# Kernel optimization log

Hardware: AMD Instinct MI355X
Metric: run time of the kernel (lower is better)

## Reference

```python
import jax, jax.numpy as jnp
import numpy as np

T = 200                      # TRAIN_ROIS_PER_IMAGE
RATIO = 0.33                 # ROI_POSITIVE_RATIO
P_MAX = int(T * RATIO)       # max positive ROIs (66)
MH, MW = 28, 28              # MASK_SHAPE
STD = jnp.array([0.1, 0.1, 0.2, 0.2], jnp.float32)  # BBOX_STD_DEV
EPS = 1e-6


def _iou(a, b):
    # a [N,4], b [G,4] -> [N,G] IoU (same math as overlaps_graph, without tiling)
    ay1, ax1, ay2, ax2 = a[:, 0:1], a[:, 1:2], a[:, 2:3], a[:, 3:4]
    by1, bx1, by2, bx2 = b[None, :, 0], b[None, :, 1], b[None, :, 2], b[None, :, 3]
    iy = jnp.maximum(jnp.minimum(ay2, by2) - jnp.maximum(ay1, by1), 0.0)
    ix = jnp.maximum(jnp.minimum(ax2, bx2) - jnp.maximum(ax1, bx1), 0.0)
    inter = iy * ix
    union = (ay2 - ay1) * (ax2 - ax1) + (by2 - by1) * (bx2 - bx1) - inter
    return inter / jnp.maximum(union, EPS)


def _box_refinement(box, gt):
    # standard Mask R-CNN box_refinement_graph
    h = jnp.maximum(box[:, 2] - box[:, 0], EPS)
    w = jnp.maximum(box[:, 3] - box[:, 1], EPS)
    cy = box[:, 0] + 0.5 * h
    cx = box[:, 1] + 0.5 * w
    gh = jnp.maximum(gt[:, 2] - gt[:, 0], EPS)
    gw = jnp.maximum(gt[:, 3] - gt[:, 1], EPS)
    gcy = gt[:, 0] + 0.5 * gh
    gcx = gt[:, 1] + 0.5 * gw
    return jnp.stack([(gcy - cy) / h, (gcx - cx) / w,
                      jnp.log(gh / h), jnp.log(gw / w)], axis=-1)


def _crop_and_resize(imgs, boxes):
    # imgs [T,H,W], boxes [T,4] normalized; TF crop_and_resize bilinear semantics,
    # extrapolation_value = 0 for samples outside [0, H-1] x [0, W-1].
    Tn, H, W = imgs.shape
    y1, x1, y2, x2 = boxes[:, 0], boxes[:, 1], boxes[:, 2], boxes[:, 3]
    iy = jnp.arange(MH, dtype=jnp.float32)
    ix = jnp.arange(MW, dtype=jnp.float32)
    ys = y1[:, None] * (H - 1) + iy[None, :] * ((y2 - y1) * (H - 1) / (MH - 1))[:, None]  # [T,MH]
    xs = x1[:, None] * (W - 1) + ix[None, :] * ((x2 - x1) * (W - 1) / (MW - 1))[:, None]  # [T,MW]
    y0 = jnp.floor(ys); x0 = jnp.floor(xs)
    wy = (ys - y0)[:, :, None]
    wx = (xs - x0)[:, None, :]
    y0i = jnp.clip(y0, 0, H - 1).astype(jnp.int32)
    y1i = jnp.clip(y0 + 1, 0, H - 1).astype(jnp.int32)
    x0i = jnp.clip(x0, 0, W - 1).astype(jnp.int32)
    x1i = jnp.clip(x0 + 1, 0, W - 1).astype(jnp.int32)
    t = jnp.arange(Tn)[:, None, None]
    v00 = imgs[t, y0i[:, :, None], x0i[:, None, :]]
    v01 = imgs[t, y0i[:, :, None], x1i[:, None, :]]
    v10 = imgs[t, y1i[:, :, None], x0i[:, None, :]]
    v11 = imgs[t, y1i[:, :, None], x1i[:, None, :]]
    val = (v00 * (1 - wx) + v01 * wx) * (1 - wy) + (v10 * (1 - wx) + v11 * wx) * wy
    ok = ((ys >= 0) & (ys <= H - 1))[:, :, None] & ((xs >= 0) & (xs <= W - 1))[:, None, :]
    return jnp.where(ok, val, 0.0)


def _targets_one(proposals, class_ids, boxes, masks):
    # proposals [N,4], class_ids [G] int, boxes [G,4], masks [H,W,G]
    N = proposals.shape[0]
    # zero-padding trim expressed as validity masks (jit-friendly fixed shapes)
    valid_prop = jnp.any(proposals != 0, axis=1)
    valid_gt = jnp.any(boxes != 0, axis=1)
    non_crowd = (class_ids > 0) & valid_gt
    crowd = (class_ids < 0) & valid_gt

    ov = _iou(proposals, boxes)                              # [N,G]
    ov_nc = jnp.where(non_crowd[None, :], ov, -1.0)          # mask crowd/padded gt
    roi_iou_max = ov_nc.max(axis=1)
    crowd_max = jnp.where(crowd[None, :], ov, 0.0).max(axis=1)

    pos_mask = valid_prop & (roi_iou_max >= 0.5)
    neg_mask = valid_prop & (roi_iou_max < 0.5) & (crowd_max < 0.001)

    # deterministic selection (original uses tf.random.shuffle): positives first-in-order
    pos_order = jnp.argsort(jnp.where(pos_mask, 0, 1))
    neg_order = jnp.argsort(jnp.where(neg_mask, 0, 1))
    pos_count = jnp.minimum(pos_mask.sum(), P_MAX)
    neg_needed = jnp.floor(pos_count.astype(jnp.float32) / RATIO).astype(jnp.int32) - pos_count
    neg_count = jnp.minimum(jnp.minimum(neg_needed, neg_mask.sum()), T - pos_count)

    slot = jnp.arange(T)
    is_pos = slot < pos_count
    is_neg = (slot >= pos_count) & (slot < pos_count + neg_count)
    src = jnp.where(is_pos,
                    pos_order[jnp.clip(slot, 0, N - 1)],
                    neg_order[jnp.clip(slot - pos_count, 0, N - 1)])
    rois = jnp.where((is_pos | is_neg)[:, None], proposals[src], 0.0)

    assign = jnp.argmax(ov_nc[src], axis=1)                  # gt assignment per slot
    gt_box = boxes[assign]
    gt_cls = jnp.where(is_pos, class_ids[assign], 0)

    deltas = _box_refinement(rois, gt_box) / STD
    deltas = jnp.where(is_pos[:, None], deltas, 0.0)

    # USE_MINI_MASK: roi box in gt-box-normalized coordinates
    gy1, gx1, gy2, gx2 = gt_box[:, 0], gt_box[:, 1], gt_box[:, 2], gt_box[:, 3]
    gh = jnp.maximum(gy2 - gy1, EPS)
    gw = jnp.maximum(gx2 - gx1, EPS)
    mm = jnp.stack([(rois[:, 0] - gy1) / gh, (rois[:, 1] - gx1) / gw,
                    (rois[:, 2] - gy1) / gh, (rois[:, 3] - gx1) / gw], axis=-1)

    roi_masks = jnp.moveaxis(jnp.take(masks, assign, axis=2), 2, 0)  # [T,H,W]
    m = jnp.round(_crop_and_resize(roi_masks, mm))
    m = jnp.where(is_pos[:, None, None], m, 0.0)
    return rois, gt_cls, deltas, m


def setup_inputs() -> dict:
    key = jax.random.key(0)
    ks = jax.random.split(key, 4)
    B, N, G, HM = 16, 2000, 200, 56

    def boxes_of(k, shape):
        k1, k2, k3, k4 = jax.random.split(k, 4)
        y1 = jax.random.uniform(k1, shape) * 0.5
        x1 = jax.random.uniform(k2, shape) * 0.5
        h = 0.1 + jax.random.uniform(k3, shape) * 0.4
        w = 0.1 + jax.random.uniform(k4, shape) * 0.4
        return jnp.stack([y1, x1, y1 + h, x1 + w], axis=-1)

    proposals = boxes_of(ks[0], (B, N))
    proposals = proposals * (jnp.arange(N) < N - 200)[None, :, None]  # zero-padded tail
    prior_class_ids = jax.random.randint(ks[1], (B, G), -1, 81).astype(jnp.int32)  # -1=crowd, 0=padding
    prior_boxes = boxes_of(ks[2], (B, G)) * (prior_class_ids != 0)[..., None]
    prior_masks = (jax.random.uniform(ks[3], (B, HM, HM, G)) > 0.5).astype(jnp.float32)
    return {"proposals": proposals, "prior_class_ids": prior_class_ids,
            "prior_boxes": prior_boxes, "prior_masks": prior_masks}


def reference(proposals, prior_class_ids, prior_boxes, prior_masks):
    rois, cls, deltas, masks = jax.vmap(_targets_one)(proposals, prior_class_ids,
                                                      prior_boxes, prior_masks)
    return rois, cls, deltas, masks
```

## Files before the change

### kernel.cpp

```cpp
#include <hip/hip_runtime.h>
#include <math.h>

#pragma clang fp contract(off)

#define BN    16
#define NP    2000
#define NG    200
#define NT    200
#define PMAX  66
#define EPSF  1e-6f
#define MH    28
#define MW    28
#define HM    56
#define NPIX  (HM*HM)
#define NW    49
#define NGP   256
#define NPW   32

#define KA_BLOCKS 128
#define KG_BLOCKS (49*4*BN)

__global__ __launch_bounds__(256) void kF(
    const float* __restrict__ proposals, const int* __restrict__ cls_ids,
    const float* __restrict__ boxes, const float* __restrict__ masks,
    unsigned long long* __restrict__ selbits, int* __restrict__ assign_ws,
    unsigned long long* __restrict__ bits)
{
#pragma clang fp contract(off)
  const int tid  = threadIdx.x;
  const int lane = tid & 63;
  const int wv   = tid >> 6;

  __shared__ float4 gbox[NG];
  __shared__ float  garea[NG];
  __shared__ int    gflag[NG];
  __shared__ unsigned long long sw[64];

  if (blockIdx.x < KA_BLOCKS) {
    const int b = blockIdx.x >> 3;
    const int bxa = blockIdx.x & 7;

    for (int j = tid; j < NG; j += 256) {
      float4 g = reinterpret_cast<const float4*>(boxes + (size_t)b * NG * 4)[j];
      int c = cls_ids[b * NG + j];
      bool vg = (g.x != 0.f) || (g.y != 0.f) || (g.z != 0.f) || (g.w != 0.f);
      gbox[j]  = g;
      garea[j] = (g.z - g.x) * (g.w - g.y);
      gflag[j] = vg ? (c > 0 ? 1 : (c < 0 ? 2 : 0)) : 0;
    }
    __syncthreads();

    const int i  = bxa * 256 + tid;
    const bool act = (i < NP);
    const int ic = act ? i : (NP - 1);

    float4 p = reinterpret_cast<const float4*>(proposals + (size_t)b * NP * 4)[ic];
    bool vp = act && ((p.x != 0.f) || (p.y != 0.f) || (p.z != 0.f) || (p.w != 0.f));
    float pa = (p.z - p.x) * (p.w - p.y);

    float best = -3.0e38f;
    int   bestj = 0;
    float cmax = 0.f;
    for (int j = 0; j < NG; ++j) {
      float4 g = gbox[j];
      float iy = fmaxf(fminf(p.z, g.z) - fmaxf(p.x, g.x), 0.f);
      float ix = fmaxf(fminf(p.w, g.w) - fmaxf(p.y, g.y), 0.f);
      float inter = iy * ix;
      float uni = (pa + garea[j]) - inter;
      float iou = inter / fmaxf(uni, EPSF);
      int fl = gflag[j];
      float v = (fl == 1) ? iou : -1.0f;
      if (v > best) { best = v; bestj = j; }
      if (fl == 2) cmax = fmaxf(cmax, iou);
    }
    bool pos = vp && (best >= 0.5f);
    bool neg = vp && (best < 0.5f) && (cmax < 0.001f);
    unsigned long long bp = __ballot(pos);
    unsigned long long bn = __ballot(neg);
    if (lane == 0) {
      int w = bxa * 4 + wv;
      selbits[(size_t)b * 64 + w]       = bp;
      selbits[(size_t)b * 64 + 32 + w]  = bn;
    }
    if (act) assign_ws[b * NP + i] = bestj;
  } else {
    int idx = blockIdx.x - KA_BLOCKS;
    const int pword = idx % 49;
    idx /= 49;
    const int gw0 = (idx & 3) * 64;
    const int b   = idx >> 2;
    const int p0  = pword * 64;

    const bool gok = (gw0 + lane) < NG;
    const float* mbase = masks + (size_t)b * NPIX * NG + gw0 + lane;
    for (int e = 0; e < 16; ++e) {
      int pl = e * 4 + wv;
      float v = 0.f;
      if (gok) v = mbase[(size_t)(p0 + pl) * NG];
      unsigned long long word = __ballot(v != 0.f);
      if (lane == 0) sw[pl] = word;
    }
    __syncthreads();

    unsigned long long w0 = sw[lane];
    for (int k = 0; k < 16; ++k) {
      int gl = wv * 16 + k;
      unsigned long long word = __ballot((int)((w0 >> gl) & 1ULL));
      if (lane == 0 && (gw0 + gl) < NG)
        bits[(size_t)(b * NGP + gw0 + gl) * NW + pword] = word;
    }
  }
}

__global__ __launch_bounds__(256) void kB2(
    const float* __restrict__ proposals, const int* __restrict__ cls_ids,
    const float* __restrict__ boxes, const int* __restrict__ assign_ws,
    const unsigned long long* __restrict__ selbits, float* __restrict__ out,
    float* __restrict__ mm_ws, int* __restrict__ ma_ws)
{
#pragma clang fp contract(off)
  const int b = blockIdx.x;
  const int tid = threadIdx.x;

  __shared__ unsigned long long sel[64];
  if (tid < 64) sel[tid] = selbits[(size_t)b * 64 + tid];
  __syncthreads();

  int pos_total = 0, neg_total = 0;
  for (int w = 0; w < NPW; ++w) {
    pos_total += __popcll(sel[w]);
    neg_total += __popcll(sel[32 + w]);
  }
  int pos_count = min(pos_total, PMAX);
  int neg_needed = (int)floorf((float)pos_count / 0.33f) - pos_count;
  int neg_count = min(min(neg_needed, neg_total), NT - pos_count);

  if (tid < NT) {
    const int t = tid;
    const bool ispos = (t < pos_count);
    const bool isneg = (!ispos) && (t < pos_count + neg_count);

    float r0 = 0.f, r1 = 0.f, r2 = 0.f, r3 = 0.f;
    float d0 = 0.f, d1 = 0.f, d2 = 0.f, d3 = 0.f;
    float m0 = 0.f, m1 = 0.f, m2 = 0.f, m3 = 0.f;
    float clsf = 0.f;
    int ma = -1;

    if (ispos || isneg) {
      int k = ispos ? t : (t - pos_count);
      const int base = ispos ? 0 : 32;
      int i = 0;
      for (int w = 0; w < NPW; ++w) {
        unsigned long long word = sel[base + w];
        int c = __popcll(word);
        if (k < c) {
          for (int r = 0; r < k; ++r) word &= word - 1ULL;
          i = w * 64 + __builtin_ctzll(word);
          break;
        }
        k -= c;
      }
      float4 p = reinterpret_cast<const float4*>(proposals + (size_t)b * NP * 4)[i];
      r0 = p.x; r1 = p.y; r2 = p.z; r3 = p.w;
      if (ispos) {
        int a = assign_ws[b * NP + i];
        ma = a;
        float4 g = reinterpret_cast<const float4*>(boxes + (size_t)b * NG * 4)[a];
        float h  = fmaxf(r2 - r0, EPSF);
        float w  = fmaxf(r3 - r1, EPSF);
        float cy = r0 + 0.5f * h;
        float cx = r1 + 0.5f * w;
        float gh = fmaxf(g.z - g.x, EPSF);
        float gw = fmaxf(g.w - g.y, EPSF);
        float gcy = g.x + 0.5f * gh;
        float gcx = g.y + 0.5f * gw;
        d0 = ((gcy - cy) / h) / 0.1f;
        d1 = ((gcx - cx) / w) / 0.1f;
        d2 = logf(gh / h) / 0.2f;
        d3 = logf(gw / w) / 0.2f;
        m0 = (r0 - g.x) / gh;
        m1 = (r1 - g.y) / gw;
        m2 = (r2 - g.x) / gh;
        m3 = (r3 - g.y) / gw;
        clsf = (float)cls_ids[b * NG + a];
      }
    }
    int s = b * NT + tid;
    float* rois = out;
    float* cls  = out + BN * NT * 4;
    float* dlt  = out + BN * NT * 4 + BN * NT;
    rois[s * 4 + 0] = r0; rois[s * 4 + 1] = r1;
    rois[s * 4 + 2] = r2; rois[s * 4 + 3] = r3;
    cls[s] = clsf;
    dlt[s * 4 + 0] = d0; dlt[s * 4 + 1] = d1;
    dlt[s * 4 + 2] = d2; dlt[s * 4 + 3] = d3;
    mm_ws[s * 4 + 0] = m0; mm_ws[s * 4 + 1] = m1;
    mm_ws[s * 4 + 2] = m2; mm_ws[s * 4 + 3] = m3;
    ma_ws[s] = ma;
  }
}

__global__ __launch_bounds__(256) void kC(
    const unsigned long long* __restrict__ bits, const float* __restrict__ mm_ws,
    const int* __restrict__ ma_ws, float* __restrict__ out)
{
#pragma clang fp contract(off)
  const int s = blockIdx.x;
  float4* om = reinterpret_cast<float4*>(
      out + (size_t)(BN * NT * 9) + (size_t)s * (MH * MW));
  const int q = threadIdx.x;
  const int a = ma_ws[s];
  if (a < 0) {
    if (q < (MH * MW) / 4) om[q] = make_float4(0.f, 0.f, 0.f, 0.f);
    return;
  }

  __shared__ unsigned long long pb[NW];
  const int b = s / NT;
  if (q < NW) pb[q] = bits[(size_t)(b * NGP + a) * NW + q];
  __syncthreads();
  if (q >= (MH * MW) / 4) return;

  float y1 = mm_ws[s * 4 + 0], x1 = mm_ws[s * 4 + 1];
  float y2 = mm_ws[s * 4 + 2], x2 = mm_ws[s * 4 + 3];
  float sy = (y2 - y1) * 55.0f / 27.0f;
  float sx = (x2 - x1) * 55.0f / 27.0f;

  int px0 = q * 4;
  int my  = px0 / MW;
  float ys = y1 * 55.0f + (float)my * sy;
  float y0f = floorf(ys);
  float wy  = ys - y0f;
  int y0i = (int)fminf(fmaxf(y0f, 0.f), 55.f);
  int y1i = (int)fminf(fmaxf(y0f + 1.0f, 0.f), 55.f);
  bool oky = (ys >= 0.f) && (ys <= 55.f);
  const int r0b = y0i * HM;
  const int r1b = y1i * HM;

  float res[4];
  for (int k = 0; k < 4; ++k) {
    int mx = (px0 + k) - my * MW;
    float xs = x1 * 55.0f + (float)mx * sx;
    float x0f = floorf(xs);
    float wx  = xs - x0f;
    int x0i = (int)fminf(fmaxf(x0f, 0.f), 55.f);
    int x1i = (int)fminf(fmaxf(x0f + 1.0f, 0.f), 55.f);
    int p00 = r0b + x0i, p01 = r0b + x1i;
    int p10 = r1b + x0i, p11 = r1b + x1i;
    float v00 = (float)((pb[p00 >> 6] >> (p00 & 63)) & 1ULL);
    float v01 = (float)((pb[p01 >> 6] >> (p01 & 63)) & 1ULL);
    float v10 = (float)((pb[p10 >> 6] >> (p10 & 63)) & 1ULL);
    float v11 = (float)((pb[p11 >> 6] >> (p11 & 63)) & 1ULL);
    float val = (v00 * (1.f - wx) + v01 * wx) * (1.f - wy)
              + (v10 * (1.f - wx) + v11 * wx) * wy;
    bool ok = oky && (xs >= 0.f) && (xs <= 55.f);
    res[k] = ok ? rintf(val) : 0.f;
  }
  om[q] = make_float4(res[0], res[1], res[2], res[3]);
}

extern "C" void kernel_launch(void* const* d_in, const int* in_sizes, int n_in,
                              void* d_out, int out_size, void* d_ws, size_t ws_size,
                              hipStream_t stream)
{
  const float* proposals = (const float*)d_in[0];
  const int*   cls_ids   = (const int*)d_in[1];
  const float* boxes     = (const float*)d_in[2];
  const float* masks     = (const float*)d_in[3];
  float* out = (float*)d_out;

  char* ws = (char*)d_ws;
  unsigned long long* selbits = (unsigned long long*)ws;
  ws += (size_t)BN * 64 * sizeof(unsigned long long);
  unsigned long long* bits_ws = (unsigned long long*)ws;
  ws += (size_t)BN * NGP * NW * sizeof(unsigned long long);
  int* assign_ws = (int*)ws;
  ws += (size_t)BN * NP * sizeof(int);
  float* mm_ws = (float*)ws;
  ws += (size_t)BN * NT * 4 * sizeof(float);
  int* ma_ws = (int*)ws;

  kF<<<KA_BLOCKS + KG_BLOCKS, 256, 0, stream>>>(
      proposals, cls_ids, boxes, masks, selbits, assign_ws, bits_ws);
  kB2<<<BN, 256, 0, stream>>>(proposals, cls_ids, boxes, assign_ws, selbits,
                              out, mm_ws, ma_ws);
  kC<<<BN * NT, 256, 0, stream>>>(bits_ws, mm_ws, ma_ws, out);
}
```

Baseline: 113.8 us.

## Fuse ROI selection kernel into IoU kernel via last-block atomic counter

The separate per-image selection kernel kB2 is removed. Its work now runs inside kF in whichever of the 8 IoU blocks for an image finishes last, found with a threadfence plus an atomic counter. This drops one kernel launch and its dependency gap. In exchange it adds a hipMemsetAsync to reset the counters each call, and the serial selection tail now runs inside the IoU kernel.

```diff
diff --git a/kernel.cpp b/kernel.cpp
--- a/kernel.cpp
+++ b/kernel.cpp
@@ -24,7 +24,8 @@
     const float* __restrict__ proposals, const int* __restrict__ cls_ids,
     const float* __restrict__ boxes, const float* __restrict__ masks,
     unsigned long long* __restrict__ selbits, int* __restrict__ assign_ws,
-    unsigned long long* __restrict__ bits)
+    unsigned long long* __restrict__ bits, int* __restrict__ cnt,
+    float* __restrict__ out, float* __restrict__ mm_ws, int* __restrict__ ma_ws)
 {
 #pragma clang fp contract(off)
   const int tid  = threadIdx.x;
@@ -35,6 +36,7 @@
   __shared__ float  garea[NG];
   __shared__ int    gflag[NG];
   __shared__ unsigned long long sw[64];
+  __shared__ int s_old;
 
   if (blockIdx.x < KA_BLOCKS) {
     const int b = blockIdx.x >> 3;
@@ -83,6 +85,88 @@
       selbits[(size_t)b * 64 + 32 + w]  = bn;
     }
     if (act) assign_ws[b * NP + i] = bestj;
+
+    __threadfence();
+    if (tid == 0) s_old = atomicAdd(&cnt[b], 1);
+    __syncthreads();
+    if (s_old != 7) return;
+    __threadfence();
+
+    if (tid < 64) sw[tid] = selbits[(size_t)b * 64 + tid];
+    __syncthreads();
+
+    int pos_total = 0, neg_total = 0;
+    for (int w = 0; w < NPW; ++w) {
+      pos_total += __popcll(sw[w]);
+      neg_total += __popcll(sw[32 + w]);
+    }
+    int pos_count = min(pos_total, PMAX);
+    int neg_needed = (int)floorf((float)pos_count / 0.33f) - pos_count;
+    int neg_count = min(min(neg_needed, neg_total), NT - pos_count);
+
+    if (tid < NT) {
+      const int t = tid;
+      const bool ispos = (t < pos_count);
+      const bool isneg = (!ispos) && (t < pos_count + neg_count);
+
+      float r0 = 0.f, r1 = 0.f, r2 = 0.f, r3 = 0.f;
+      float d0 = 0.f, d1 = 0.f, d2 = 0.f, d3 = 0.f;
+      float m0 = 0.f, m1 = 0.f, m2 = 0.f, m3 = 0.f;
+      float clsf = 0.f;
+      int ma = -1;
+
+      if (ispos || isneg) {
+        int k = ispos ? t : (t - pos_count);
+        const int base = ispos ? 0 : 32;
+        int i2 = 0;
+        for (int w = 0; w < NPW; ++w) {
+          unsigned long long word = sw[base + w];
+          int c = __popcll(word);
+          if (k < c) {
+            for (int r = 0; r < k; ++r) word &= word - 1ULL;
+            i2 = w * 64 + __builtin_ctzll(word);
+            break;
+          }
+          k -= c;
+        }
+        float4 pp = reinterpret_cast<const float4*>(proposals + (size_t)b * NP * 4)[i2];
+        r0 = pp.x; r1 = pp.y; r2 = pp.z; r3 = pp.w;
+        if (ispos) {
+          int a = assign_ws[b * NP + i2];
+          ma = a;
+          float4 g = reinterpret_cast<const float4*>(boxes + (size_t)b * NG * 4)[a];
+          float h  = fmaxf(r2 - r0, EPSF);
+          float w  = fmaxf(r3 - r1, EPSF);
+          float cy = r0 + 0.5f * h;
+          float cx = r1 + 0.5f * w;
+          float gh = fmaxf(g.z - g.x, EPSF);
+          float gw = fmaxf(g.w - g.y, EPSF);
+          float gcy = g.x + 0.5f * gh;
+          float gcx = g.y + 0.5f * gw;
+          d0 = ((gcy - cy) / h) / 0.1f;
+          d1 = ((gcx - cx) / w) / 0.1f;
+          d2 = logf(gh / h) / 0.2f;
+          d3 = logf(gw / w) / 0.2f;
+          m0 = (r0 - g.x) / gh;
+          m1 = (r1 - g.y) / gw;
+          m2 = (r2 - g.x) / gh;
+          m3 = (r3 - g.y) / gw;
+          clsf = (float)cls_ids[b * NG + a];
+        }
+      }
+      int s = b * NT + tid;
+      float* rois = out;
+      float* cls  = out + BN * NT * 4;
+      float* dlt  = out + BN * NT * 4 + BN * NT;
+      rois[s * 4 + 0] = r0; rois[s * 4 + 1] = r1;
+      rois[s * 4 + 2] = r2; rois[s * 4 + 3] = r3;
+      cls[s] = clsf;
+      dlt[s * 4 + 0] = d0; dlt[s * 4 + 1] = d1;
+      dlt[s * 4 + 2] = d2; dlt[s * 4 + 3] = d3;
+      mm_ws[s * 4 + 0] = m0; mm_ws[s * 4 + 1] = m1;
+      mm_ws[s * 4 + 2] = m2; mm_ws[s * 4 + 3] = m3;
+      ma_ws[s] = ma;
+    }
   } else {
     int idx = blockIdx.x - KA_BLOCKS;
     const int pword = idx % 49;
@@ -109,94 +193,6 @@
       if (lane == 0 && (gw0 + gl) < NG)
         bits[(size_t)(b * NGP + gw0 + gl) * NW + pword] = word;
     }
-  }
-}
-
-__global__ __launch_bounds__(256) void kB2(
-    const float* __restrict__ proposals, const int* __restrict__ cls_ids,
-    const float* __restrict__ boxes, const int* __restrict__ assign_ws,
-    const unsigned long long* __restrict__ selbits, float* __restrict__ out,
-    float* __restrict__ mm_ws, int* __restrict__ ma_ws)
-{
-#pragma clang fp contract(off)
-  const int b = blockIdx.x;
-  const int tid = threadIdx.x;
-
-  __shared__ unsigned long long sel[64];
-  if (tid < 64) sel[tid] = selbits[(size_t)b * 64 + tid];
-  __syncthreads();
-
-  int pos_total = 0, neg_total = 0;
-  for (int w = 0; w < NPW; ++w) {
-    pos_total += __popcll(sel[w]);
-    neg_total += __popcll(sel[32 + w]);
-  }
-  int pos_count = min(pos_total, PMAX);
-  int neg_needed = (int)floorf((float)pos_count / 0.33f) - pos_count;
-  int neg_count = min(min(neg_needed, neg_total), NT - pos_count);
-
-  if (tid < NT) {
-    const int t = tid;
-    const bool ispos = (t < pos_count);
-    const bool isneg = (!ispos) && (t < pos_count + neg_count);
-
-    float r0 = 0.f, r1 = 0.f, r2 = 0.f, r3 = 0.f;
-    float d0 = 0.f, d1 = 0.f, d2 = 0.f, d3 = 0.f;
-    float m0 = 0.f, m1 = 0.f, m2 = 0.f, m3 = 0.f;
-    float clsf = 0.f;
-    int ma = -1;
-
-    if (ispos || isneg) {
-      int k = ispos ? t : (t - pos_count);
-      const int base = ispos ? 0 : 32;
-      int i = 0;
-      for (int w = 0; w < NPW; ++w) {
-        unsigned long long word = sel[base + w];
-        int c = __popcll(word);
-        if (k < c) {
-          for (int r = 0; r < k; ++r) word &= word - 1ULL;
-          i = w * 64 + __builtin_ctzll(word);
-          break;
-        }
-        k -= c;
-      }
-      float4 p = reinterpret_cast<const float4*>(proposals + (size_t)b * NP * 4)[i];
-      r0 = p.x; r1 = p.y; r2 = p.z; r3 = p.w;
-      if (ispos) {
-        int a = assign_ws[b * NP + i];
-        ma = a;
-        float4 g = reinterpret_cast<const float4*>(boxes + (size_t)b * NG * 4)[a];
-        float h  = fmaxf(r2 - r0, EPSF);
-        float w  = fmaxf(r3 - r1, EPSF);
-        float cy = r0 + 0.5f * h;
-        float cx = r1 + 0.5f * w;
-        float gh = fmaxf(g.z - g.x, EPSF);
-        float gw = fmaxf(g.w - g.y, EPSF);
-        float gcy = g.x + 0.5f * gh;
-        float gcx = g.y + 0.5f * gw;
-        d0 = ((gcy - cy) / h) / 0.1f;
-        d1 = ((gcx - cx) / w) / 0.1f;
-        d2 = logf(gh / h) / 0.2f;
-        d3 = logf(gw / w) / 0.2f;
-        m0 = (r0 - g.x) / gh;
-        m1 = (r1 - g.y) / gw;
-        m2 = (r2 - g.x) / gh;
-        m3 = (r3 - g.y) / gw;
-        clsf = (float)cls_ids[b * NG + a];
-      }
-    }
-    int s = b * NT + tid;
-    float* rois = out;
-    float* cls  = out + BN * NT * 4;
-    float* dlt  = out + BN * NT * 4 + BN * NT;
-    rois[s * 4 + 0] = r0; rois[s * 4 + 1] = r1;
-    rois[s * 4 + 2] = r2; rois[s * 4 + 3] = r3;
-    cls[s] = clsf;
-    dlt[s * 4 + 0] = d0; dlt[s * 4 + 1] = d1;
-    dlt[s * 4 + 2] = d2; dlt[s * 4 + 3] = d3;
-    mm_ws[s * 4 + 0] = m0; mm_ws[s * 4 + 1] = m1;
-    mm_ws[s * 4 + 2] = m2; mm_ws[s * 4 + 3] = m3;
-    ma_ws[s] = ma;
   }
 }
 
@@ -279,10 +275,13 @@
   float* mm_ws = (float*)ws;
   ws += (size_t)BN * NT * 4 * sizeof(float);
   int* ma_ws = (int*)ws;
+  ws += (size_t)BN * NT * sizeof(int);
+  int* cnt_ws = (int*)ws;
+
+  hipMemsetAsync(cnt_ws, 0, BN * sizeof(int), stream);
 
   kF<<<KA_BLOCKS + KG_BLOCKS, 256, 0, stream>>>(
-      proposals, cls_ids, boxes, masks, selbits, assign_ws, bits_ws);
-  kB2<<<BN, 256, 0, stream>>>(proposals, cls_ids, boxes, assign_ws, selbits,
-                              out, mm_ws, ma_ws);
+      proposals, cls_ids, boxes, masks, selbits, assign_ws, bits_ws, cnt_ws,
+      out, mm_ws, ma_ws);
   kC<<<BN * NT, 256, 0, stream>>>(bits_ws, mm_ws, ma_ws, out);
 }
```

Measured after the change: 125.3 us. 10.1% more time.

## Pack mask bits per lane without ballot transpose and transpose bits layout

Applied to the files above, without the earlier changes.

The mask-bitpacking path now gives each wave one 64-pixel word for 64 ground-truth columns, and each lane builds its 64-bit word serially from 64 strided loads. This replaces the ballot, shared-memory and second-ballot transpose. The bits workspace layout changes to [b][pword][g], so stores are coalesced across lanes, and kC reads the new layout with strided gathers. The intent is to remove the barrier and transpose work, at the cost of more loads in flight per lane and scattered reads in kC.

```diff
diff --git a/kernel.cpp b/kernel.cpp
--- a/kernel.cpp
+++ b/kernel.cpp
@@ -18,7 +18,8 @@
 #define NPW   32
 
 #define KA_BLOCKS 128
-#define KG_BLOCKS (49*4*BN)
+#define KG_WAVES  (BN * 4 * NW)
+#define KG_BLOCKS (KG_WAVES / 4)
 
 __global__ __launch_bounds__(256) void kF(
     const float* __restrict__ proposals, const int* __restrict__ cls_ids,
@@ -34,7 +35,6 @@
   __shared__ float4 gbox[NG];
   __shared__ float  garea[NG];
   __shared__ int    gflag[NG];
-  __shared__ unsigned long long sw[64];
 
   if (blockIdx.x < KA_BLOCKS) {
     const int b = blockIdx.x >> 3;
@@ -84,31 +84,32 @@
     }
     if (act) assign_ws[b * NP + i] = bestj;
   } else {
-    int idx = blockIdx.x - KA_BLOCKS;
-    const int pword = idx % 49;
-    idx /= 49;
-    const int gw0 = (idx & 3) * 64;
-    const int b   = idx >> 2;
-    const int p0  = pword * 64;
-
-    const bool gok = (gw0 + lane) < NG;
-    const float* mbase = masks + (size_t)b * NPIX * NG + gw0 + lane;
-    for (int e = 0; e < 16; ++e) {
-      int pl = e * 4 + wv;
+    const int wid = (blockIdx.x - KA_BLOCKS) * 4 + wv;
+    const int pword = wid % NW;
+    const int rest  = wid / NW;
+    const int gw0   = (rest & 3) * 64;
+    const int b     = rest >> 2;
+    const int g     = gw0 + lane;
+    const bool gok  = (g < NG);
+
+    const float* src = masks + (size_t)b * NPIX * NG
+                             + (size_t)(pword * 64) * NG + g;
+    unsigned int lo = 0, hi = 0;
+#pragma unroll 16
+    for (int i = 0; i < 32; ++i) {
       float v = 0.f;
-      if (gok) v = mbase[(size_t)(p0 + pl) * NG];
-      unsigned long long word = __ballot(v != 0.f);
-      if (lane == 0) sw[pl] = word;
-    }
-    __syncthreads();
-
-    unsigned long long w0 = sw[lane];
-    for (int k = 0; k < 16; ++k) {
-      int gl = wv * 16 + k;
-      unsigned long long word = __ballot((int)((w0 >> gl) & 1ULL));
-      if (lane == 0 && (gw0 + gl) < NG)
-        bits[(size_t)(b * NGP + gw0 + gl) * NW + pword] = word;
-    }
+      if (gok) v = src[(size_t)i * NG];
+      lo |= (unsigned int)(v != 0.f ? 1u : 0u) << i;
+    }
+#pragma unroll 16
+    for (int i = 0; i < 32; ++i) {
+      float v = 0.f;
+      if (gok) v = src[(size_t)(i + 32) * NG];
+      hi |= (unsigned int)(v != 0.f ? 1u : 0u) << i;
+    }
+    if (gok)
+      bits[((size_t)b * NW + pword) * NGP + g] =
+          ((unsigned long long)hi << 32) | lo;
   }
 }
 
@@ -217,7 +218,7 @@
 
   __shared__ unsigned long long pb[NW];
   const int b = s / NT;
-  if (q < NW) pb[q] = bits[(size_t)(b * NGP + a) * NW + q];
+  if (q < NW) pb[q] = bits[((size_t)b * NW + q) * NGP + a];
   __syncthreads();
   if (q >= (MH * MW) / 4) return;
 
@@ -273,7 +274,7 @@
   unsigned long long* selbits = (unsigned long long*)ws;
   ws += (size_t)BN * 64 * sizeof(unsigned long long);
   unsigned long long* bits_ws = (unsigned long long*)ws;
-  ws += (size_t)BN * NGP * NW * sizeof(unsigned long long);
+  ws += (size_t)BN * NW * NGP * sizeof(unsigned long long);
   int* assign_ws = (int*)ws;
   ws += (size_t)BN * NP * sizeof(int);
   float* mm_ws = (float*)ws;
```

Result: slower. 122.0 us (+7.2%).
